# Kernel optimization log

Hardware: AMD Instinct MI355X
Metric: run time of the kernel (lower is better)

The kernel has to match this reference:

```python
import jax, jax.numpy as jnp
import numpy as np

K_LEN, I_LEN, DIM = 1024, 8192, 128


def setup_inputs() -> dict:
    key = jax.random.key(0)
    k1, k2 = jax.random.split(key)
    kernel = jax.random.normal(k1, (K_LEN, DIM), dtype=jnp.float32)
    x = jax.random.normal(k2, (I_LEN, DIM), dtype=jnp.float32)
    return {"kernel": kernel, "x": x}


def _cost_matrix(kernel, x):
    # squared Euclidean pairwise distances, (K, I), via GEMM form
    k2 = jnp.sum(kernel * kernel, axis=-1)  # (K,)
    x2 = jnp.sum(x * x, axis=-1)            # (I,)
    c = k2[:, None] + x2[None, :] - 2.0 * (kernel @ x.T)
    return jnp.maximum(c, 0.0)


def _acc_matrix(c):
    # DTW DP: D[i,j] = c[i,j] + min(D[i-1,j-1], D[i-1,j], D[i,j-1])
    # Row recurrence solved per-row with a (min,+) prefix scan:
    #   e[j] = min(D_prev[j-1], D_prev[j]) + c[j]   (e[0] = D_prev[0] + c[0])
    #   D[j] = S[j] + cummin(e - S),  S = cumsum(c_row)
    row0 = jnp.cumsum(c[0])

    def step(prev, c_row):
        m = jnp.concatenate([prev[:1], jnp.minimum(prev[:-1], prev[1:])])
        e = m + c_row
        S = jnp.cumsum(c_row)
        row = S + jax.lax.cummin(e - S)
        return row, row

    _, rows = jax.lax.scan(step, row0, c[1:])
    return jnp.concatenate([row0[None, :], rows], axis=0)  # (K, I)


def _backtrack(D):
    # tslearn-style backtracking from (K-1, I-1) to (0, 0).
    # Candidate order [diag, up, left]; argmin ties pick first (diag),
    # matching numpy.argmin used by tslearn. Out-of-range -> +inf border.
    K, I = D.shape
    Dp = jnp.full((K + 1, I + 1), jnp.inf, dtype=D.dtype).at[1:, 1:].set(D)
    L = K + I - 1  # max possible path length

    def step(carry, _):
        k, i, fin = carry
        emit = (k, i, jnp.logical_not(fin))
        fin2 = fin | ((k == 0) & (i == 0))
        cand = jnp.stack([Dp[k, i], Dp[k, i + 1], Dp[k + 1, i]])
        a = jnp.argmin(cand)
        nk = jnp.where(fin2, k, k - (a != 2).astype(k.dtype))
        ni = jnp.where(fin2, i, i - (a != 1).astype(i.dtype))
        return (nk, ni, fin2), emit

    init = (jnp.int32(K - 1), jnp.int32(I - 1), jnp.bool_(False))
    _, (ks, iss, valid) = jax.lax.scan(step, init, None, length=L)
    return ks, iss, valid


def reference(kernel, x):
    # Path search uses detached tensors in the original module.
    c = jax.lax.stop_gradient(_cost_matrix(kernel, x))
    D = _acc_matrix(c)
    ks, iss, valid = _backtrack(D)
    # sum of squared diffs along the optimal alignment path (gather + reduce)
    d2 = jnp.sum((kernel[ks] - x[iss]) ** 2, axis=-1)  # (L,)
    return jnp.sum(jnp.where(valid, d2, 0.0))
```

## Files before the change

kernel.cpp:

```cpp
#include <hip/hip_runtime.h>
#include <hip/hip_bf16.h>

typedef unsigned short ushort_t;
typedef unsigned int uint_t;

#define KL 1024
#define IL 8192
#define DIMV 128
#define NS 16
#define NB 258
#define NIT2 270
#define SSH (8256*64)
#define GATE 416
#define INF __builtin_inff()

typedef __attribute__((ext_vector_type(8))) short v8s;
typedef __attribute__((ext_vector_type(4))) float v4f;

__global__ __launch_bounds__(256) void knorms(
    const float* __restrict__ kern, const float* __restrict__ xx,
    float* __restrict__ x2, float* __restrict__ k2, int* __restrict__ flags) {
  if (blockIdx.x == 0 && threadIdx.x < NS) flags[threadIdx.x] = 0;
  const int lane = threadIdx.x & 63;
  const int row = blockIdx.x * 4 + (threadIdx.x >> 6);
  const float* src;
  float* dst;
  if (row < IL) { src = xx + (size_t)row * DIMV; dst = x2 + row; }
  else          { src = kern + (size_t)(row - IL) * DIMV; dst = k2 + (row - IL); }
  float2 v = *(const float2*)(src + lane * 2);
  float ss = v.x * v.x + v.y * v.y;
  #pragma unroll
  for (int off = 32; off > 0; off >>= 1) ss += __shfl_down(ss, off, 64);
  if (lane == 0) *dst = ss;
}

__device__ __forceinline__ v8s pack_bf16x8(float4 a, float4 b) {
  union { unsigned int u[4]; v8s v; } r;
  union { __hip_bfloat162 h; unsigned int u; } t;
  t.h = __float22bfloat162_rn(make_float2(a.x, a.y)); r.u[0] = t.u;
  t.h = __float22bfloat162_rn(make_float2(a.z, a.w)); r.u[1] = t.u;
  t.h = __float22bfloat162_rn(make_float2(b.x, b.y)); r.u[2] = t.u;
  t.h = __float22bfloat162_rn(make_float2(b.z, b.w)); r.u[3] = t.u;
  return r.v;
}

__global__ __launch_bounds__(256) void kgemm(
    const float* __restrict__ kern, const float* __restrict__ xx,
    const float* __restrict__ x2, const float* __restrict__ k2,
    ushort_t* __restrict__ c_h) {
  __shared__ float ctile[64 * 64];
  const int T = threadIdx.x;
  const int w = T >> 6;
  const int lane = T & 63;
  const int lo = lane & 15;
  const int hi = lane >> 4;
  const int i0 = blockIdx.x * 64;
  const int s  = blockIdx.y;
  const int kr0 = s * 64;

  v4f acc[4] = {};
  #pragma unroll
  for (int ks = 0; ks < 4; ks++) {
    const int k = ks * 32 + hi * 8;
    const float* bp = xx + (size_t)(i0 + w * 16 + lo) * DIMV + k;
    v8s bf = pack_bf16x8(*(const float4*)bp, *(const float4*)(bp + 4));
    #pragma unroll
    for (int rt = 0; rt < 4; rt++) {
      const float* ap = kern + (size_t)(kr0 + rt * 16 + lo) * DIMV + k;
      v8s af = pack_bf16x8(*(const float4*)ap, *(const float4*)(ap + 4));
      acc[rt] = __builtin_amdgcn_mfma_f32_16x16x32_bf16(af, bf, acc[rt], 0, 0, 0);
    }
  }
  const float x2v = x2[i0 + w * 16 + lo];
  const int n_local = w * 16 + lo;
  #pragma unroll
  for (int rt = 0; rt < 4; rt++) {
    float4 k2f = *(const float4*)&k2[kr0 + rt * 16 + hi * 4];
    #pragma unroll
    for (int q = 0; q < 4; q++) {
      const int m_local = rt * 16 + hi * 4 + q;
      float cval = fmaxf((&k2f.x)[q] + x2v - 2.f * acc[rt][q], 0.f);
      ctile[n_local * 64 + ((m_local + 2 * n_local) & 63)] = cval;
    }
  }
  __syncthreads();
  _Float16* ob = (_Float16*)(c_h + (size_t)s * SSH);
  #pragma unroll
  for (int q = 0; q < 32; q++) {
    int tt = w + q * 4;
    int di = tt - lane;
    if (tt <= 126 && di >= 0 && di < 64) {
      int t = i0 + tt;
      int tp = t >> 1;
      ob[(((size_t)(tp >> 4) * 1024) + lane * 16 + (tp & 15)) * 2 + (t & 1)] =
          (_Float16)ctile[di * 64 + ((lane + 2 * di) & 63)];
    }
  }
}

__device__ __forceinline__ float dpp_wave_shr1(float oldv, float src) {
  return __int_as_float(__builtin_amdgcn_update_dpp(
      __float_as_int(oldv), __float_as_int(src), 0x138, 0xF, 0xF, false));
}

__global__ __launch_bounds__(320, 1) void kdp(
    const ushort_t* __restrict__ c_h, float* __restrict__ bound,
    int* __restrict__ flags, float* __restrict__ out) {
  __shared__ __align__(16) float ring[4 * 4 * 32];
  __shared__ __align__(16) float feed[4 * 32];
  const int g = blockIdx.x;
  const int wv = threadIdx.x >> 6;
  const int lane = threadIdx.x & 63;
  const int sb = g * 4;

  float Dcur = INF, Dul = INF;
  int fchk = 0, fpend = 0;
  float rfeed = INF;
  const float* bin = bound + (size_t)(sb > 0 ? sb - 1 : 0) * IL;
  float* bout3 = bound + (size_t)(sb + 3) * IL;

  const uint4* cbase4 = (const uint4*)((const uint_t*)c_h +
      (size_t)(sb + (wv < 4 ? wv : 0)) * (SSH / 2) + lane * 16);

  uint4 Pb[4], Qb[4];

  if (wv < 4) {
    Pb[0] = cbase4[0]; Pb[1] = cbase4[1]; Pb[2] = cbase4[2]; Pb[3] = cbase4[3];
    if (g == 0 && wv == 0 && lane == 0) Dcur = 0.f;
  } else {
    if (g > 0) {
      int f;
      do { f = __hip_atomic_load(&flags[sb - 1], __ATOMIC_RELAXED, __HIP_MEMORY_SCOPE_AGENT); } while (f < GATE);
      fchk = f; fpend = f;
      if (lane < 32) {
        feed[lane]      = __hip_atomic_load(&bin[lane],      __ATOMIC_RELAXED, __HIP_MEMORY_SCOPE_AGENT);
        feed[32 + lane] = __hip_atomic_load(&bin[32 + lane], __ATOMIC_RELAXED, __HIP_MEMORY_SCOPE_AGENT);
        rfeed           = __hip_atomic_load(&bin[64 + lane], __ATOMIC_RELAXED, __HIP_MEMORY_SCOPE_AGENT);
      }
    } else {
      if (lane < 32) { feed[lane] = INF; feed[32+lane] = INF; feed[64+lane] = INF; feed[96+lane] = INF; }
    }
  }
  __syncthreads();

  auto body = [&](int i, uint4 (&cur)[4], uint4 (&nxt)[4]) {
    if (wv < 4) {
      const int W = i - 3 * wv;
      int Wn = W + 1; Wn = Wn < 0 ? 0 : (Wn > NB - 1 ? NB - 1 : Wn);
      const uint4* sp = cbase4 + (size_t)Wn * 256;
      if (W >= 0 && W < NB) {
        const float* fb = (wv == 0) ? &feed[(W & 3) * 32]
                                    : &ring[(wv - 1) * 128 + (W & 3) * 32];
        float fv[32];
        #pragma unroll
        for (int q = 0; q < 8; q++) {
          float4 f4 = *(const float4*)(fb + q * 4);
          fv[4 * q]     = f4.x; fv[4 * q + 1] = f4.y;
          fv[4 * q + 2] = f4.z; fv[4 * q + 3] = f4.w;
        }
        float cvv[32];
        #pragma unroll
        for (int q = 0; q < 4; q++) {
          const uint4 v = cur[q];
          union { uint_t u; _Float16 h[2]; } cu;
          cu.u = v.x; cvv[8*q+0] = (float)cu.h[0]; cvv[8*q+1] = (float)cu.h[1];
          cu.u = v.y; cvv[8*q+2] = (float)cu.h[0]; cvv[8*q+3] = (float)cu.h[1];
          cu.u = v.z; cvv[8*q+4] = (float)cu.h[0]; cvv[8*q+5] = (float)cu.h[1];
          cu.u = v.w; cvv[8*q+6] = (float)cu.h[0]; cvv[8*q+7] = (float)cu.h[1];
        }
        nxt[0] = sp[0]; nxt[1] = sp[1]; nxt[2] = sp[2]; nxt[3] = sp[3];
        float bb[32];
        if (W >= 2 && W < 256) {
          #pragma unroll
          for (int tt = 0; tt < 32; tt++) {
            float Dup = dpp_wave_shr1(fv[tt], Dcur);
            float m1 = fminf(Dul, Dcur);
            Dcur = cvv[tt] + fminf(m1, Dup);
            Dul = Dup;
            bb[tt] = Dcur;
          }
        } else {
          const int t0 = W * 32;
          #pragma unroll
          for (int tt = 0; tt < 32; tt++) {
            const int t = t0 + tt;
            float Dup = dpp_wave_shr1(fv[tt], Dcur);
            float m1 = fminf(Dul, Dcur);
            float Dnew = cvv[tt] + fminf(m1, Dup);
            const bool alo = (t >= lane);
            const bool ahi = (t - lane < IL);
            if (alo) Dul = Dup;
            if (alo && ahi) Dcur = Dnew;
            bb[tt] = Dcur;
          }
        }
        if (lane == 63) {
          const int base2 = wv * 128 + (((W - 2) & 3) << 5);
          const int base1 = wv * 128 + (((W - 1) & 3) << 5);
          if (W >= 2) {
            #pragma unroll
            for (int tt = 0; tt < 31; tt++) ring[base2 + tt + 1] = bb[tt];
          }
          if (W >= 1) ring[base1] = bb[31];
        }
      } else {
        nxt[0] = sp[0]; nxt[1] = sp[1]; nxt[2] = sp[2]; nxt[3] = sp[3];
      }
      asm volatile("s_waitcnt lgkmcnt(0)" ::: "memory");
      __builtin_amdgcn_s_barrier();
    } else {
      asm volatile("s_waitcnt vmcnt(0)" ::: "memory");
      if (g > 0) {
        if (fpend > fchk) fchk = fpend;
        const int Fw = i + 2;
        if (Fw >= 2 && Fw <= 255 && lane < 32) feed[(Fw & 3) * 32 + lane] = rfeed;
        const int Fl = i + 3;
        if (Fl <= 255) {
          const int need = 32 * (Fl + 1);
          if (fchk < need) {
            int f;
            do { f = __hip_atomic_load(&flags[sb - 1], __ATOMIC_RELAXED, __HIP_MEMORY_SCOPE_AGENT); } while (f < need);
            fchk = f;
          }
          if (lane < 32)
            rfeed = __hip_atomic_load(&bin[32 * Fl + lane], __ATOMIC_RELAXED, __HIP_MEMORY_SCOPE_AGENT);
        }
        fpend = __hip_atomic_load(&flags[sb - 1], __ATOMIC_RELAXED, __HIP_MEMORY_SCOPE_AGENT);
      }
      if (g < 3) {
        const int E = i - 12;
        if (E >= 0 && E < 256 && lane < 32) {
          float bv2 = ring[3 * 128 + (E & 3) * 32 + lane];
          __hip_atomic_store(&bout3[32 * E + lane], bv2, __ATOMIC_RELAXED, __HIP_MEMORY_SCOPE_AGENT);
        }
        const int Ep = i - 13;
        if (Ep >= 0 && Ep < 256 && lane == 0)
          __hip_atomic_store(&flags[sb + 3], 32 * Ep + 32, __ATOMIC_RELAXED, __HIP_MEMORY_SCOPE_AGENT);
      }
      asm volatile("s_waitcnt lgkmcnt(0)" ::: "memory");
      __builtin_amdgcn_s_barrier();
    }
  };

  for (int i = 0; i < NIT2; i += 2) {
    body(i, Pb, Qb);
    body(i + 1, Qb, Pb);
  }

  asm volatile("s_waitcnt vmcnt(0)" ::: "memory");
  if (g == 3 && wv == 3 && lane == 63) out[0] = Dcur;
}

extern "C" void kernel_launch(void* const* d_in, const int* in_sizes, int n_in,
                              void* d_out, int out_size, void* d_ws, size_t ws_size,
                              hipStream_t stream) {
  const float* kern = (const float*)d_in[0];
  const float* xx   = (const float*)d_in[1];
  char* ws = (char*)d_ws;
  const size_t OFF_X2 = (size_t)NS * SSH * 2;
  const size_t OFF_K2 = OFF_X2 + (size_t)IL * 4;
  const size_t OFF_BD = OFF_K2 + (size_t)KL * 4;
  const size_t OFF_FL = OFF_BD + (size_t)NS * IL * 4;
  ushort_t* c_h  = (ushort_t*)ws;
  float* x2    = (float*)(ws + OFF_X2);
  float* k2    = (float*)(ws + OFF_K2);
  float* bnd   = (float*)(ws + OFF_BD);
  int*   flags = (int*)(ws + OFF_FL);

  knorms<<<(IL + KL) / 4, 256, 0, stream>>>(kern, xx, x2, k2, flags);
  kgemm<<<dim3(IL / 64, NS), 256, 0, stream>>>(kern, xx, x2, k2, c_h);
  kdp<<<4, 320, 0, stream>>>(c_h, bnd, flags, (float*)d_out);
}
```

Before: 445.1 us.

## Process two 32-column chunks per barrier step in DTW wavefront pipeline

Measured after the change: 427.2 us. 4.0% less time.

```diff
diff --git a/kernel.cpp b/kernel.cpp
--- a/kernel.cpp
+++ b/kernel.cpp
@@ -9,9 +9,10 @@
 #define DIMV 128
 #define NS 16
 #define NB 258
-#define NIT2 270
+#define NP 129
+#define NIT2 140
 #define SSH (8256*64)
-#define GATE 416
+#define GATE 512
 #define INF __builtin_inff()
 
 typedef __attribute__((ext_vector_type(8))) short v8s;
@@ -106,8 +107,8 @@
 __global__ __launch_bounds__(320, 1) void kdp(
     const ushort_t* __restrict__ c_h, float* __restrict__ bound,
     int* __restrict__ flags, float* __restrict__ out) {
-  __shared__ __align__(16) float ring[4 * 4 * 32];
-  __shared__ __align__(16) float feed[4 * 32];
+  __shared__ __align__(16) float ring[4 * 8 * 32];
+  __shared__ __align__(16) float feed[8 * 32];
   const int g = blockIdx.x;
   const int wv = threadIdx.x >> 6;
   const int lane = threadIdx.x & 63;
@@ -122,89 +123,108 @@
   const uint4* cbase4 = (const uint4*)((const uint_t*)c_h +
       (size_t)(sb + (wv < 4 ? wv : 0)) * (SSH / 2) + lane * 16);
 
-  uint4 Pb[4], Qb[4];
+  uint4 Pb[8], Qb[8];
 
   if (wv < 4) {
-    Pb[0] = cbase4[0]; Pb[1] = cbase4[1]; Pb[2] = cbase4[2]; Pb[3] = cbase4[3];
+    #pragma unroll
+    for (int q = 0; q < 4; q++) { Pb[q] = cbase4[q]; Pb[4 + q] = cbase4[256 + q]; }
     if (g == 0 && wv == 0 && lane == 0) Dcur = 0.f;
   } else {
     if (g > 0) {
       int f;
       do { f = __hip_atomic_load(&flags[sb - 1], __ATOMIC_RELAXED, __HIP_MEMORY_SCOPE_AGENT); } while (f < GATE);
       fchk = f; fpend = f;
-      if (lane < 32) {
-        feed[lane]      = __hip_atomic_load(&bin[lane],      __ATOMIC_RELAXED, __HIP_MEMORY_SCOPE_AGENT);
-        feed[32 + lane] = __hip_atomic_load(&bin[32 + lane], __ATOMIC_RELAXED, __HIP_MEMORY_SCOPE_AGENT);
-        rfeed           = __hip_atomic_load(&bin[64 + lane], __ATOMIC_RELAXED, __HIP_MEMORY_SCOPE_AGENT);
-      }
+      feed[lane]      = __hip_atomic_load(&bin[lane],       __ATOMIC_RELAXED, __HIP_MEMORY_SCOPE_AGENT);
+      feed[64 + lane] = __hip_atomic_load(&bin[64 + lane],  __ATOMIC_RELAXED, __HIP_MEMORY_SCOPE_AGENT);
+      rfeed           = __hip_atomic_load(&bin[128 + lane], __ATOMIC_RELAXED, __HIP_MEMORY_SCOPE_AGENT);
     } else {
-      if (lane < 32) { feed[lane] = INF; feed[32+lane] = INF; feed[64+lane] = INF; feed[96+lane] = INF; }
+      feed[lane] = INF; feed[64 + lane] = INF; feed[128 + lane] = INF; feed[192 + lane] = INF;
     }
   }
   __syncthreads();
 
-  auto body = [&](int i, uint4 (&cur)[4], uint4 (&nxt)[4]) {
+  auto chain32 = [&](int W, const float (&fv)[32], const float (&cvv)[32], float (&bb)[32]) {
+    if (W >= 2 && W < 256) {
+      #pragma unroll
+      for (int tt = 0; tt < 32; tt++) {
+        float Dup = dpp_wave_shr1(fv[tt], Dcur);
+        float m1 = fminf(Dul, Dcur);
+        Dcur = cvv[tt] + fminf(m1, Dup);
+        Dul = Dup;
+        bb[tt] = Dcur;
+      }
+    } else {
+      const int t0 = W * 32;
+      #pragma unroll
+      for (int tt = 0; tt < 32; tt++) {
+        const int t = t0 + tt;
+        float Dup = dpp_wave_shr1(fv[tt], Dcur);
+        float m1 = fminf(Dul, Dcur);
+        float Dnew = cvv[tt] + fminf(m1, Dup);
+        const bool alo = (t >= lane);
+        const bool ahi = (t - lane < IL);
+        if (alo) Dul = Dup;
+        if (alo && ahi) Dcur = Dnew;
+        bb[tt] = Dcur;
+      }
+    }
+    if (lane == 63) {
+      const int base2 = wv * 256 + (((W - 2) & 7) << 5);
+      const int base1 = wv * 256 + (((W - 1) & 7) << 5);
+      if (W >= 2) {
+        #pragma unroll
+        for (int tt = 0; tt < 31; tt++) ring[base2 + tt + 1] = bb[tt];
+      }
+      if (W >= 1) ring[base1] = bb[31];
+    }
+  };
+
+  auto body = [&](int i, uint4 (&cur)[8], uint4 (&nxt)[8]) {
     if (wv < 4) {
-      const int W = i - 3 * wv;
-      int Wn = W + 1; Wn = Wn < 0 ? 0 : (Wn > NB - 1 ? NB - 1 : Wn);
-      const uint4* sp = cbase4 + (size_t)Wn * 256;
-      if (W >= 0 && W < NB) {
-        const float* fb = (wv == 0) ? &feed[(W & 3) * 32]
-                                    : &ring[(wv - 1) * 128 + (W & 3) * 32];
-        float fv[32];
+      const int V = i - 3 * wv;
+      int Vn = V + 1; Vn = Vn < 0 ? 0 : (Vn > NP - 1 ? NP - 1 : Vn);
+      const uint4* sp = cbase4 + (size_t)Vn * 512;
+      if (V >= 0 && V < NP) {
+        const int W0 = 2 * V;
+        const float* fb = (wv == 0) ? &feed[(V & 3) << 6]
+                                    : &ring[(wv - 1) * 256 + ((V & 3) << 6)];
+        float fv0[32], fv1[32];
         #pragma unroll
         for (int q = 0; q < 8; q++) {
-          float4 f4 = *(const float4*)(fb + q * 4);
-          fv[4 * q]     = f4.x; fv[4 * q + 1] = f4.y;
-          fv[4 * q + 2] = f4.z; fv[4 * q + 3] = f4.w;
-        }
-        float cvv[32];
+          float4 a = *(const float4*)(fb + q * 4);
+          fv0[4*q] = a.x; fv0[4*q+1] = a.y; fv0[4*q+2] = a.z; fv0[4*q+3] = a.w;
+          float4 b = *(const float4*)(fb + 32 + q * 4);
+          fv1[4*q] = b.x; fv1[4*q+1] = b.y; fv1[4*q+2] = b.z; fv1[4*q+3] = b.w;
+        }
+        float cvv0[32];
         #pragma unroll
         for (int q = 0; q < 4; q++) {
           const uint4 v = cur[q];
           union { uint_t u; _Float16 h[2]; } cu;
-          cu.u = v.x; cvv[8*q+0] = (float)cu.h[0]; cvv[8*q+1] = (float)cu.h[1];
-          cu.u = v.y; cvv[8*q+2] = (float)cu.h[0]; cvv[8*q+3] = (float)cu.h[1];
-          cu.u = v.z; cvv[8*q+4] = (float)cu.h[0]; cvv[8*q+5] = (float)cu.h[1];
-          cu.u = v.w; cvv[8*q+6] = (float)cu.h[0]; cvv[8*q+7] = (float)cu.h[1];
-        }
-        nxt[0] = sp[0]; nxt[1] = sp[1]; nxt[2] = sp[2]; nxt[3] = sp[3];
-        float bb[32];
-        if (W >= 2 && W < 256) {
-          #pragma unroll
-          for (int tt = 0; tt < 32; tt++) {
-            float Dup = dpp_wave_shr1(fv[tt], Dcur);
-            float m1 = fminf(Dul, Dcur);
-            Dcur = cvv[tt] + fminf(m1, Dup);
-            Dul = Dup;
-            bb[tt] = Dcur;
-          }
-        } else {
-          const int t0 = W * 32;
-          #pragma unroll
-          for (int tt = 0; tt < 32; tt++) {
-            const int t = t0 + tt;
-            float Dup = dpp_wave_shr1(fv[tt], Dcur);
-            float m1 = fminf(Dul, Dcur);
-            float Dnew = cvv[tt] + fminf(m1, Dup);
-            const bool alo = (t >= lane);
-            const bool ahi = (t - lane < IL);
-            if (alo) Dul = Dup;
-            if (alo && ahi) Dcur = Dnew;
-            bb[tt] = Dcur;
-          }
-        }
-        if (lane == 63) {
-          const int base2 = wv * 128 + (((W - 2) & 3) << 5);
-          const int base1 = wv * 128 + (((W - 1) & 3) << 5);
-          if (W >= 2) {
-            #pragma unroll
-            for (int tt = 0; tt < 31; tt++) ring[base2 + tt + 1] = bb[tt];
-          }
-          if (W >= 1) ring[base1] = bb[31];
-        }
+          cu.u = v.x; cvv0[8*q+0] = (float)cu.h[0]; cvv0[8*q+1] = (float)cu.h[1];
+          cu.u = v.y; cvv0[8*q+2] = (float)cu.h[0]; cvv0[8*q+3] = (float)cu.h[1];
+          cu.u = v.z; cvv0[8*q+4] = (float)cu.h[0]; cvv0[8*q+5] = (float)cu.h[1];
+          cu.u = v.w; cvv0[8*q+6] = (float)cu.h[0]; cvv0[8*q+7] = (float)cu.h[1];
+        }
+        #pragma unroll
+        for (int q = 0; q < 4; q++) { nxt[q] = sp[q]; nxt[4 + q] = sp[256 + q]; }
+        float bb0[32];
+        chain32(W0, fv0, cvv0, bb0);
+        float cvv1[32];
+        #pragma unroll
+        for (int q = 0; q < 4; q++) {
+          const uint4 v = cur[4 + q];
+          union { uint_t u; _Float16 h[2]; } cu;
+          cu.u = v.x; cvv1[8*q+0] = (float)cu.h[0]; cvv1[8*q+1] = (float)cu.h[1];
+          cu.u = v.y; cvv1[8*q+2] = (float)cu.h[0]; cvv1[8*q+3] = (float)cu.h[1];
+          cu.u = v.z; cvv1[8*q+4] = (float)cu.h[0]; cvv1[8*q+5] = (float)cu.h[1];
+          cu.u = v.w; cvv1[8*q+6] = (float)cu.h[0]; cvv1[8*q+7] = (float)cu.h[1];
+        }
+        float bb1[32];
+        chain32(W0 + 1, fv1, cvv1, bb1);
       } else {
-        nxt[0] = sp[0]; nxt[1] = sp[1]; nxt[2] = sp[2]; nxt[3] = sp[3];
+        #pragma unroll
+        for (int q = 0; q < 4; q++) { nxt[q] = sp[q]; nxt[4 + q] = sp[256 + q]; }
       }
       asm volatile("s_waitcnt lgkmcnt(0)" ::: "memory");
       __builtin_amdgcn_s_barrier();
@@ -213,29 +233,28 @@
       if (g > 0) {
         if (fpend > fchk) fchk = fpend;
         const int Fw = i + 2;
-        if (Fw >= 2 && Fw <= 255 && lane < 32) feed[(Fw & 3) * 32 + lane] = rfeed;
+        if (Fw >= 2 && Fw <= 127) feed[((Fw & 3) << 6) + lane] = rfeed;
         const int Fl = i + 3;
-        if (Fl <= 255) {
-          const int need = 32 * (Fl + 1);
+        if (Fl <= 127) {
+          const int need = 64 * (Fl + 1);
           if (fchk < need) {
             int f;
             do { f = __hip_atomic_load(&flags[sb - 1], __ATOMIC_RELAXED, __HIP_MEMORY_SCOPE_AGENT); } while (f < need);
             fchk = f;
           }
-          if (lane < 32)
-            rfeed = __hip_atomic_load(&bin[32 * Fl + lane], __ATOMIC_RELAXED, __HIP_MEMORY_SCOPE_AGENT);
+          rfeed = __hip_atomic_load(&bin[64 * Fl + lane], __ATOMIC_RELAXED, __HIP_MEMORY_SCOPE_AGENT);
         }
         fpend = __hip_atomic_load(&flags[sb - 1], __ATOMIC_RELAXED, __HIP_MEMORY_SCOPE_AGENT);
       }
       if (g < 3) {
-        const int E = i - 12;
-        if (E >= 0 && E < 256 && lane < 32) {
-          float bv2 = ring[3 * 128 + (E & 3) * 32 + lane];
-          __hip_atomic_store(&bout3[32 * E + lane], bv2, __ATOMIC_RELAXED, __HIP_MEMORY_SCOPE_AGENT);
-        }
-        const int Ep = i - 13;
-        if (Ep >= 0 && Ep < 256 && lane == 0)
-          __hip_atomic_store(&flags[sb + 3], 32 * Ep + 32, __ATOMIC_RELAXED, __HIP_MEMORY_SCOPE_AGENT);
+        const int E = i - 11;
+        if (E >= 0 && E <= 127) {
+          float bv2 = ring[3 * 256 + ((E & 3) << 6) + lane];
+          __hip_atomic_store(&bout3[64 * E + lane], bv2, __ATOMIC_RELAXED, __HIP_MEMORY_SCOPE_AGENT);
+        }
+        const int Ep = i - 12;
+        if (Ep >= 0 && Ep <= 127 && lane == 0)
+          __hip_atomic_store(&flags[sb + 3], 64 * Ep + 64, __ATOMIC_RELAXED, __HIP_MEMORY_SCOPE_AGENT);
       }
       asm volatile("s_waitcnt lgkmcnt(0)" ::: "memory");
       __builtin_amdgcn_s_barrier();
```
